# Optimization experiments

Measured on AMD Instinct MI355X. Metric: run time of the kernel, lower is better.

The kernel has to match this reference:

```python
import jax, jax.numpy as jnp
import numpy as np

HIDDEN = 1024
NUM_HEADS = 16
D_HEAD = HIDDEN // NUM_HEADS  # 64
SEQ = 2048
BATCH = 2


def setup_inputs() -> dict:
    key = jax.random.key(0)
    kx, kw, kb = jax.random.split(key, 3)
    x = jax.random.normal(kx, (SEQ, BATCH, HIDDEN), dtype=jnp.float32)
    W = jax.random.normal(kw, (3 * HIDDEN, HIDDEN), dtype=jnp.float32) * 0.02
    b = jax.random.normal(kb, (3 * HIDDEN,), dtype=jnp.float32) * 0.02
    return {"x": x, "W": W, "b": b}


def reference(x, W, b):
    # x: (S, B, H) seq-first, as in the torch module
    S, B, _ = x.shape
    qkv = jnp.einsum('sbh,oh->sbo', x, W) + b  # (S, B, 3*H)
    # torch views 3*hidden as (num_heads, 3, d_head): per-head-interleaved QKV
    qkv = qkv.reshape(S, B, NUM_HEADS, 3, D_HEAD)
    qkv = jnp.transpose(qkv, (2, 1, 0, 3, 4))  # (nh, B, S, 3, d)
    q, k, v = qkv[..., 0, :], qkv[..., 1, :], qkv[..., 2, :]  # each (nh, B, S, d)
    scale = 1.0 / np.sqrt(D_HEAD).astype(np.float32)
    scores = jnp.einsum('hbqd,hbkd->hbqk', q, k) * scale  # (nh, B, S, S)
    attn = jax.nn.softmax(scores, axis=-1)
    out = jnp.einsum('hbqk,hbkd->hbqd', attn, v)  # (nh, B, S, d)
    out = jnp.transpose(out, (2, 1, 0, 3)).reshape(S, B, HIDDEN)
    return out
```

## Files before the change

### kernel.cpp

```cpp
#include <hip/hip_runtime.h>
#include <hip/hip_bf16.h>


typedef __hip_bfloat16 bf16;
typedef __bf16 bfr;
typedef __attribute__((ext_vector_type(8))) __bf16 bf16x8;
typedef __attribute__((ext_vector_type(4))) __bf16 bf16x4;
typedef __attribute__((ext_vector_type(4))) float f32x4;

#define S_SEQ  2048
#define HID    1024
#define OUT3   3072
#define NROWS  4096
#define LSTR   72

__global__ __launch_bounds__(256) void cast_bf16_kernel(
    const float* __restrict__ src, bfr* __restrict__ dst)
{
    int gid = blockIdx.x * 256 + threadIdx.x;
    const float4* s4 = (const float4*)src;
    float4 a = s4[(size_t)gid * 2];
    float4 b = s4[(size_t)gid * 2 + 1];
    bf16x8 v;
    v[0] = (bfr)a.x; v[1] = (bfr)a.y; v[2] = (bfr)a.z; v[3] = (bfr)a.w;
    v[4] = (bfr)b.x; v[5] = (bfr)b.y; v[6] = (bfr)b.z; v[7] = (bfr)b.w;
    *(bf16x8*)(dst + (size_t)gid * 8) = v;
}

__device__ __forceinline__ void gload_lds16(const void* g, void* l) {
    __builtin_amdgcn_global_load_lds(
        (const __attribute__((address_space(1))) unsigned int*)g,
        (__attribute__((address_space(3))) unsigned int*)l, 16, 0, 0);
}

__global__ __launch_bounds__(256, 3) void qkv_gemm_mfma(
    const bfr* __restrict__ Xb, const bfr* __restrict__ Wb,
    const float* __restrict__ bias,
    bfr* __restrict__ qb, bfr* __restrict__ kb, bfr* __restrict__ vtb)
{
    __shared__ __attribute__((aligned(16))) bfr As[128 * 64];
    __shared__ __attribute__((aligned(16))) bfr Bs[128 * 64];

    const int o0 = blockIdx.x * 128;
    const int r0 = blockIdx.y * 128;
    const int tid = threadIdx.x;
    const int lane = tid & 63;
    const int w = tid >> 6;
    const int l15 = lane & 15;
    const int quad = lane >> 4;
    const int m0 = (w & 1) * 64;
    const int n0 = (w >> 1) * 64;

    f32x4 acc[4][4];
#pragma unroll
    for (int mi = 0; mi < 4; mi++)
#pragma unroll
        for (int ni = 0; ni < 4; ni++) acc[mi][ni] = {0.f, 0.f, 0.f, 0.f};

    for (int k0 = 0; k0 < HID; k0 += 64) {
#pragma unroll
        for (int i = 0; i < 4; i++) {
            int c = i * 256 + tid;
            int row = c >> 3, c8 = c & 7;
            gload_lds16(Xb + (size_t)(r0 + row) * HID + k0 + c8 * 8, As + c * 8);
            gload_lds16(Wb + (size_t)(o0 + row) * HID + k0 + c8 * 8, Bs + c * 8);
        }
        __syncthreads();

#pragma unroll
        for (int ks = 0; ks < 2; ks++) {
            bf16x8 af[4], bfg[4];
#pragma unroll
            for (int mi = 0; mi < 4; mi++)
                af[mi] = *(const bf16x8*)(As + (m0 + mi * 16 + l15) * 64 + ks * 32 + quad * 8);
#pragma unroll
            for (int ni = 0; ni < 4; ni++)
                bfg[ni] = *(const bf16x8*)(Bs + (n0 + ni * 16 + l15) * 64 + ks * 32 + quad * 8);
#pragma unroll
            for (int mi = 0; mi < 4; mi++)
#pragma unroll
                for (int ni = 0; ni < 4; ni++)
                    acc[mi][ni] = __builtin_amdgcn_mfma_f32_16x16x32_bf16(
                        af[mi], bfg[ni], acc[mi][ni], 0, 0, 0);
        }
        __syncthreads();
    }

#pragma unroll
    for (int ni = 0; ni < 4; ni++) {
        int cb = o0 + n0 + ni * 16;
        int h = cb / 192;
        int rem = cb % 192;
        int t = rem >> 6;
        int d = (rem & 63) + l15;
        float bv = bias[cb + l15];
#pragma unroll
        for (int mi = 0; mi < 4; mi++) {
#pragma unroll
            for (int r = 0; r < 4; r++) {
                int gr = r0 + m0 + mi * 16 + quad * 4 + r;
                int s = gr >> 1, b = gr & 1;
                int hb = h * 2 + b;
                float val = acc[mi][ni][r] + bv;
                if (t == 0)
                    qb[((size_t)hb * S_SEQ + s) * 64 + d] = (bfr)(val * 0.125f);
                else if (t == 1)
                    kb[((size_t)hb * S_SEQ + s) * 64 + d] = (bfr)val;
                else
                    vtb[((size_t)hb * 64 + d) * S_SEQ + s] = (bfr)val;
            }
        }
    }
}

__global__ __launch_bounds__(256, 4) void attn2_kernel(
    const bfr* __restrict__ qb, const bfr* __restrict__ kb,
    const bfr* __restrict__ vtb, float* __restrict__ out)
{
    __shared__ __attribute__((aligned(16))) bfr Ks [64 * LSTR];
    __shared__ __attribute__((aligned(16))) bfr Vts[64 * LSTR];
    __shared__ __attribute__((aligned(16))) bfr Ptq[64 * LSTR];

    const int qt = blockIdx.x;
    const int hb = blockIdx.y;
    const int h = hb >> 1, b = hb & 1;
    const int tid = threadIdx.x;
    const int lane = tid & 63;
    const int w = tid >> 6;
    const int l15 = lane & 15;
    const int quad = lane >> 4;
    const size_t hboff = (size_t)hb * S_SEQ * 64;

    const int qrow = qt * 64 + 16 * w + l15;
    bf16x8 qf[2];
    qf[0] = *(const bf16x8*)(qb + hboff + (size_t)qrow * 64 + quad * 8);
    qf[1] = *(const bf16x8*)(qb + hboff + (size_t)qrow * 64 + quad * 8 + 32);

    f32x4 Oacc[4];
#pragma unroll
    for (int mt = 0; mt < 4; mt++) Oacc[mt] = {0.f, 0.f, 0.f, 0.f};
    float m_st = -1e30f, l_st = 0.f;

    for (int kt = 0; kt < 32; kt++) {
#pragma unroll
        for (int p = 0; p < 2; p++) {
            int c = tid + p * 256;
            int row = c >> 3, c8 = c & 7;
            *(bf16x8*)(Ks + row * LSTR + c8 * 8) =
                *(const bf16x8*)(kb + hboff + (size_t)(kt * 64 + row) * 64 + c8 * 8);
            *(bf16x8*)(Vts + row * LSTR + c8 * 8) =
                *(const bf16x8*)(vtb + hboff + (size_t)row * S_SEQ + kt * 64 + c8 * 8);
        }
        __syncthreads();

        f32x4 sc[4];
#pragma unroll
        for (int mt = 0; mt < 4; mt++) sc[mt] = {0.f, 0.f, 0.f, 0.f};
#pragma unroll
        for (int k0 = 0; k0 < 2; k0++) {
#pragma unroll
            for (int mt = 0; mt < 4; mt++) {
                bf16x8 kf = *(const bf16x8*)(Ks + (mt * 16 + l15) * LSTR + quad * 8 + 32 * k0);
                sc[mt] = __builtin_amdgcn_mfma_f32_16x16x32_bf16(kf, qf[k0], sc[mt], 0, 0, 0);
            }
        }

        float lm = sc[0][0];
#pragma unroll
        for (int mt = 0; mt < 4; mt++)
#pragma unroll
            for (int r = 0; r < 4; r++) lm = fmaxf(lm, sc[mt][r]);
        lm = fmaxf(lm, __shfl_xor(lm, 16));
        lm = fmaxf(lm, __shfl_xor(lm, 32));
        float mnew = fmaxf(m_st, lm);
        float alpha = __expf(m_st - mnew);
        m_st = mnew;

        float rs = 0.f;
#pragma unroll
        for (int mt = 0; mt < 4; mt++) {
            bf16x4 pk;
#pragma unroll
            for (int r = 0; r < 4; r++) {
                float pv = __expf(sc[mt][r] - mnew);
                rs += pv;
                pk[r] = (bfr)pv;
            }
            *(bf16x4*)(Ptq + (16 * w + l15) * LSTR + mt * 16 + quad * 4) = pk;
        }
        rs += __shfl_xor(rs, 16);
        rs += __shfl_xor(rs, 32);
        l_st = l_st * alpha + rs;
#pragma unroll
        for (int mt = 0; mt < 4; mt++)
#pragma unroll
            for (int r = 0; r < 4; r++) Oacc[mt][r] *= alpha;

#pragma unroll
        for (int k0 = 0; k0 < 2; k0++) {
            bf16x8 pf = *(const bf16x8*)(Ptq + (16 * w + l15) * LSTR + quad * 8 + 32 * k0);
#pragma unroll
            for (int mt = 0; mt < 4; mt++) {
                bf16x8 vf = *(const bf16x8*)(Vts + (mt * 16 + l15) * LSTR + quad * 8 + 32 * k0);
                Oacc[mt] = __builtin_amdgcn_mfma_f32_16x16x32_bf16(vf, pf, Oacc[mt], 0, 0, 0);
            }
        }
        __syncthreads();
    }

    float inv = 1.0f / l_st;
    float* orow = out + ((size_t)qrow * 2 + b) * HID + h * 64;
#pragma unroll
    for (int mt = 0; mt < 4; mt++) {
        float4 o4;
        o4.x = Oacc[mt][0] * inv;
        o4.y = Oacc[mt][1] * inv;
        o4.z = Oacc[mt][2] * inv;
        o4.w = Oacc[mt][3] * inv;
        *(float4*)(orow + mt * 16 + quad * 4) = o4;
    }
}

extern "C" void kernel_launch(void* const* d_in, const int* in_sizes, int n_in,
                              void* d_out, int out_size, void* d_ws, size_t ws_size,
                              hipStream_t stream) {
    const float* X    = (const float*)d_in[0];
    const float* W    = (const float*)d_in[1];
    const float* bias = (const float*)d_in[2];
    float* out = (float*)d_out;

    bfr* qb  = (bfr*)d_ws;
    bfr* kb  = qb + (size_t)32 * S_SEQ * 64;
    bfr* vtb = kb + (size_t)32 * S_SEQ * 64;

    bfr* Xb = (bfr*)d_out;
    bfr* Wb = Xb + (size_t)NROWS * HID;

    cast_bf16_kernel<<<NROWS * HID / (256 * 8), 256, 0, stream>>>(X, Xb);
    cast_bf16_kernel<<<OUT3 * HID / (256 * 8), 256, 0, stream>>>(W, Wb);

    dim3 g1(OUT3 / 128, NROWS / 128);
    qkv_gemm_mfma<<<g1, 256, 0, stream>>>(Xb, Wb, bias, qb, kb, vtb);

    dim3 g2(S_SEQ / 64, 32);
    attn2_kernel<<<g2, 256, 0, stream>>>(qb, kb, vtb, out);
}
```

Before: 193.0 us.

## Process two 16-row query tiles per wave to reuse K/V tiles

Each attention block now covers 128 query rows instead of 64, with every wave handling two 16-row query tiles against the same K/V tile in shared memory. This halves the K/V load and sync overhead per query and interleaves independent MFMA chains. The cost is more registers, a lower occupancy hint, and half as many blocks, which may underfill the GPU.

```diff
diff --git a/kernel.cpp b/kernel.cpp
--- a/kernel.cpp
+++ b/kernel.cpp
@@ -113,13 +113,13 @@
     }
 }
 
-__global__ __launch_bounds__(256, 4) void attn2_kernel(
+__global__ __launch_bounds__(256, 2) void attn3_kernel(
     const bfr* __restrict__ qb, const bfr* __restrict__ kb,
     const bfr* __restrict__ vtb, float* __restrict__ out)
 {
     __shared__ __attribute__((aligned(16))) bfr Ks [64 * LSTR];
     __shared__ __attribute__((aligned(16))) bfr Vts[64 * LSTR];
-    __shared__ __attribute__((aligned(16))) bfr Ptq[64 * LSTR];
+    __shared__ __attribute__((aligned(16))) bfr Ptq[128 * LSTR];
 
     const int qt = blockIdx.x;
     const int hb = blockIdx.y;
@@ -131,15 +131,21 @@
     const int quad = lane >> 4;
     const size_t hboff = (size_t)hb * S_SEQ * 64;
 
-    const int qrow = qt * 64 + 16 * w + l15;
-    bf16x8 qf[2];
-    qf[0] = *(const bf16x8*)(qb + hboff + (size_t)qrow * 64 + quad * 8);
-    qf[1] = *(const bf16x8*)(qb + hboff + (size_t)qrow * 64 + quad * 8 + 32);
-
-    f32x4 Oacc[4];
-#pragma unroll
-    for (int mt = 0; mt < 4; mt++) Oacc[mt] = {0.f, 0.f, 0.f, 0.f};
-    float m_st = -1e30f, l_st = 0.f;
+    const int qrow0 = qt * 128 + 32 * w + l15;
+    bf16x8 qf[2][2];
+#pragma unroll
+    for (int qn = 0; qn < 2; qn++)
+#pragma unroll
+        for (int k0 = 0; k0 < 2; k0++)
+            qf[qn][k0] = *(const bf16x8*)(qb + hboff +
+                (size_t)(qrow0 + 16 * qn) * 64 + quad * 8 + 32 * k0);
+
+    f32x4 Oacc[2][4];
+#pragma unroll
+    for (int qn = 0; qn < 2; qn++)
+#pragma unroll
+        for (int mt = 0; mt < 4; mt++) Oacc[qn][mt] = {0.f, 0.f, 0.f, 0.f};
+    float m_st[2] = {-1e30f, -1e30f}, l_st[2] = {0.f, 0.f};
 
     for (int kt = 0; kt < 32; kt++) {
 #pragma unroll
@@ -153,71 +159,88 @@
         }
         __syncthreads();
 
-        f32x4 sc[4];
-#pragma unroll
-        for (int mt = 0; mt < 4; mt++) sc[mt] = {0.f, 0.f, 0.f, 0.f};
+        f32x4 sc[2][4];
+#pragma unroll
+        for (int qn = 0; qn < 2; qn++)
+#pragma unroll
+            for (int mt = 0; mt < 4; mt++) sc[qn][mt] = {0.f, 0.f, 0.f, 0.f};
 #pragma unroll
         for (int k0 = 0; k0 < 2; k0++) {
 #pragma unroll
             for (int mt = 0; mt < 4; mt++) {
                 bf16x8 kf = *(const bf16x8*)(Ks + (mt * 16 + l15) * LSTR + quad * 8 + 32 * k0);
-                sc[mt] = __builtin_amdgcn_mfma_f32_16x16x32_bf16(kf, qf[k0], sc[mt], 0, 0, 0);
-            }
-        }
-
-        float lm = sc[0][0];
-#pragma unroll
-        for (int mt = 0; mt < 4; mt++)
-#pragma unroll
-            for (int r = 0; r < 4; r++) lm = fmaxf(lm, sc[mt][r]);
-        lm = fmaxf(lm, __shfl_xor(lm, 16));
-        lm = fmaxf(lm, __shfl_xor(lm, 32));
-        float mnew = fmaxf(m_st, lm);
-        float alpha = __expf(m_st - mnew);
-        m_st = mnew;
-
-        float rs = 0.f;
-#pragma unroll
-        for (int mt = 0; mt < 4; mt++) {
-            bf16x4 pk;
-#pragma unroll
-            for (int r = 0; r < 4; r++) {
-                float pv = __expf(sc[mt][r] - mnew);
-                rs += pv;
-                pk[r] = (bfr)pv;
-            }
-            *(bf16x4*)(Ptq + (16 * w + l15) * LSTR + mt * 16 + quad * 4) = pk;
-        }
-        rs += __shfl_xor(rs, 16);
-        rs += __shfl_xor(rs, 32);
-        l_st = l_st * alpha + rs;
-#pragma unroll
-        for (int mt = 0; mt < 4; mt++)
-#pragma unroll
-            for (int r = 0; r < 4; r++) Oacc[mt][r] *= alpha;
+#pragma unroll
+                for (int qn = 0; qn < 2; qn++)
+                    sc[qn][mt] = __builtin_amdgcn_mfma_f32_16x16x32_bf16(
+                        kf, qf[qn][k0], sc[qn][mt], 0, 0, 0);
+            }
+        }
+
+#pragma unroll
+        for (int qn = 0; qn < 2; qn++) {
+            float lm = sc[qn][0][0];
+#pragma unroll
+            for (int mt = 0; mt < 4; mt++)
+#pragma unroll
+                for (int r = 0; r < 4; r++) lm = fmaxf(lm, sc[qn][mt][r]);
+            lm = fmaxf(lm, __shfl_xor(lm, 16));
+            lm = fmaxf(lm, __shfl_xor(lm, 32));
+            float mnew = fmaxf(m_st[qn], lm);
+            float alpha = __expf(m_st[qn] - mnew);
+            m_st[qn] = mnew;
+
+            float rs = 0.f;
+#pragma unroll
+            for (int mt = 0; mt < 4; mt++) {
+                bf16x4 pk;
+#pragma unroll
+                for (int r = 0; r < 4; r++) {
+                    float pv = __expf(sc[qn][mt][r] - mnew);
+                    rs += pv;
+                    pk[r] = (bfr)pv;
+                }
+                *(bf16x4*)(Ptq + (32 * w + 16 * qn + l15) * LSTR + mt * 16 + quad * 4) = pk;
+            }
+            rs += __shfl_xor(rs, 16);
+            rs += __shfl_xor(rs, 32);
+            l_st[qn] = l_st[qn] * alpha + rs;
+#pragma unroll
+            for (int mt = 0; mt < 4; mt++)
+#pragma unroll
+                for (int r = 0; r < 4; r++) Oacc[qn][mt][r] *= alpha;
+        }
 
 #pragma unroll
         for (int k0 = 0; k0 < 2; k0++) {
-            bf16x8 pf = *(const bf16x8*)(Ptq + (16 * w + l15) * LSTR + quad * 8 + 32 * k0);
+            bf16x8 pf[2];
+#pragma unroll
+            for (int qn = 0; qn < 2; qn++)
+                pf[qn] = *(const bf16x8*)(Ptq + (32 * w + 16 * qn + l15) * LSTR + quad * 8 + 32 * k0);
 #pragma unroll
             for (int mt = 0; mt < 4; mt++) {
                 bf16x8 vf = *(const bf16x8*)(Vts + (mt * 16 + l15) * LSTR + quad * 8 + 32 * k0);
-                Oacc[mt] = __builtin_amdgcn_mfma_f32_16x16x32_bf16(vf, pf, Oacc[mt], 0, 0, 0);
-            }
-        }
-        __syncthreads();
-    }
-
-    float inv = 1.0f / l_st;
-    float* orow = out + ((size_t)qrow * 2 + b) * HID + h * 64;
-#pragma unroll
-    for (int mt = 0; mt < 4; mt++) {
-        float4 o4;
-        o4.x = Oacc[mt][0] * inv;
-        o4.y = Oacc[mt][1] * inv;
-        o4.z = Oacc[mt][2] * inv;
-        o4.w = Oacc[mt][3] * inv;
-        *(float4*)(orow + mt * 16 + quad * 4) = o4;
+#pragma unroll
+                for (int qn = 0; qn < 2; qn++)
+                    Oacc[qn][mt] = __builtin_amdgcn_mfma_f32_16x16x32_bf16(
+                        vf, pf[qn], Oacc[qn][mt], 0, 0, 0);
+            }
+        }
+        __syncthreads();
+    }
+
+#pragma unroll
+    for (int qn = 0; qn < 2; qn++) {
+        float inv = 1.0f / l_st[qn];
+        float* orow = out + ((size_t)(qrow0 + 16 * qn) * 2 + b) * HID + h * 64;
+#pragma unroll
+        for (int mt = 0; mt < 4; mt++) {
+            float4 o4;
+            o4.x = Oacc[qn][mt][0] * inv;
+            o4.y = Oacc[qn][mt][1] * inv;
+            o4.z = Oacc[qn][mt][2] * inv;
+            o4.w = Oacc[qn][mt][3] * inv;
+            *(float4*)(orow + mt * 16 + quad * 4) = o4;
+        }
     }
 }
 
@@ -242,6 +265,6 @@
     dim3 g1(OUT3 / 128, NROWS / 128);
     qkv_gemm_mfma<<<g1, 256, 0, stream>>>(Xb, Wb, bias, qb, kb, vtb);
 
-    dim3 g2(S_SEQ / 64, 32);
-    attn2_kernel<<<g2, 256, 0, stream>>>(qb, kb, vtb, out);
-}
+    dim3 g2(S_SEQ / 128, 32);
+    attn3_kernel<<<g2, 256, 0, stream>>>(qb, kb, vtb, out);
+}
```

Result: slower. 203.8 us (+5.6%).
